# Performance work log

Hardware: AMD Instinct MI355X
Metric: run time of the kernel (lower is better)

The kernel has to match this reference:

```python
import jax, jax.numpy as jnp
import numpy as np

GROUPS = 8
EPS = 1e-3  # keras GroupNormalization default epsilon


def group_norm(x, gamma, beta):
    # x: [B, H, W, C], channels-last, normalize over (H, W, C//G) per group
    B, H, W, C = x.shape
    g = x.reshape(B, H, W, GROUPS, C // GROUPS)
    mean = g.mean(axis=(1, 2, 4), keepdims=True)
    var = g.var(axis=(1, 2, 4), keepdims=True)
    g = (g - mean) * jax.lax.rsqrt(var + EPS)
    return g.reshape(B, H, W, C) * gamma + beta


def setup_inputs() -> dict:
    key = jax.random.key(0)
    ks = jax.random.split(key, 6)
    B, H, W, C = 4, 64, 64, 256
    s = 1.0 / np.sqrt(C)
    return {
        "x": jax.random.normal(ks[0], (B, H, W, C), jnp.float32),
        "gn_gamma": jnp.ones((C,), jnp.float32),
        "gn_beta": jnp.zeros((C,), jnp.float32),
        "Wq": jax.random.normal(ks[1], (C, C), jnp.float32) * s,
        "bq": jnp.zeros((C,), jnp.float32),
        "Wk": jax.random.normal(ks[2], (C, C), jnp.float32) * s,
        "bk": jnp.zeros((C,), jnp.float32),
        "Wv": jax.random.normal(ks[3], (C, C), jnp.float32) * s,
        "bv": jnp.zeros((C,), jnp.float32),
        "Wp": jax.random.normal(ks[4], (C, C), jnp.float32) * s,
        "bp": jnp.zeros((C,), jnp.float32),
    }


def reference(x, gn_gamma, gn_beta, Wq, bq, Wk, bk, Wv, bv, Wp, bp):
    B, H, W, C = x.shape
    scale = jnp.float32(C) ** -0.5
    xn = group_norm(x, gn_gamma, gn_beta)  # note: residual uses NORMALIZED input (as in source)
    xf = xn.reshape(B, H * W, C)           # flatten spatial -> [B, N, C]
    q = xf @ Wq + bq
    k = xf @ Wk + bk
    v = xf @ Wv + bv
    attn = jnp.einsum('bnc,bmc->bnm', q, k) * scale  # [B, N, N]
    attn = jax.nn.softmax(attn, axis=-1)
    out = jnp.einsum('bnm,bmc->bnc', attn, v)
    out = out @ Wp + bp
    return xn + out.reshape(B, H, W, C)
```

## Files before the change

kernel.cpp:

```cpp
#include <hip/hip_runtime.h>
#include <hip/hip_bf16.h>

typedef __bf16 bf16x8 __attribute__((ext_vector_type(8)));
typedef __bf16 bf16x4 __attribute__((ext_vector_type(4)));
typedef float f32x4 __attribute__((ext_vector_type(4)));
typedef float f32x16 __attribute__((ext_vector_type(16)));

#define MFMA16(a,b,c) __builtin_amdgcn_mfma_f32_16x16x32_bf16((a),(b),(c),0,0,0)
#define MFMA32(a,b,c) __builtin_amdgcn_mfma_f32_32x32x16_bf16((a),(b),(c),0,0,0)

__device__ __forceinline__ void gload_lds16(const void* g, void* l) {
    __builtin_amdgcn_global_load_lds((const __attribute__((address_space(1))) unsigned int*)g,
                                     (__attribute__((address_space(3))) unsigned int*)l, 16, 0, 0);
}

__global__ __launch_bounds__(256) void gn_stats1(const float* __restrict__ x,
                                                 float* __restrict__ pstats) {
    int blk = blockIdx.x;
    int bg = blk >> 4, sl = blk & 15;
    int b = bg >> 3, g = bg & 7;
    const float* base = x + ((size_t)b * 4096 + sl * 256) * 256 + g * 32;
    float s = 0.f, s2 = 0.f;
    for (int i = threadIdx.x; i < 2048; i += 256) {
        int pos = i >> 3, f4 = i & 7;
        float4 v = *(const float4*)(base + (size_t)pos * 256 + f4 * 4);
        s  += v.x + v.y + v.z + v.w;
        s2 += v.x * v.x + v.y * v.y + v.z * v.z + v.w * v.w;
    }
    for (int off = 32; off; off >>= 1) {
        s  += __shfl_down(s, off);
        s2 += __shfl_down(s2, off);
    }
    __shared__ float red[8];
    int wave = threadIdx.x >> 6, lane = threadIdx.x & 63;
    if (lane == 0) { red[wave] = s; red[4 + wave] = s2; }
    __syncthreads();
    if (threadIdx.x == 0) {
        pstats[blk * 2]     = red[0] + red[1] + red[2] + red[3];
        pstats[blk * 2 + 1] = red[4] + red[5] + red[6] + red[7];
    }
}

__global__ void gn_stats2(const float* __restrict__ pstats, float* __restrict__ stats) {
    int bg = threadIdx.x;
    if (bg < 32) {
        float S = 0.f, S2 = 0.f;
        for (int sl = 0; sl < 16; sl++) {
            S  += pstats[(bg * 16 + sl) * 2];
            S2 += pstats[(bg * 16 + sl) * 2 + 1];
        }
        const float invN = 1.f / 131072.f;
        float mean = S * invN;
        float var = S2 * invN - mean * mean;
        stats[bg * 2] = mean;
        stats[bg * 2 + 1] = rsqrtf(var + 1e-3f);
    }
}

__global__ __launch_bounds__(256) void gn_norm(const float* __restrict__ x,
                                               const float* __restrict__ gamma,
                                               const float* __restrict__ beta,
                                               const float* __restrict__ stats,
                                               float* __restrict__ xn_f32,
                                               __bf16* __restrict__ xn_bf) {
    size_t idx = (size_t)blockIdx.x * 256 + threadIdx.x;
    int c4 = (int)(idx & 63);
    int row = (int)(idx >> 6);
    int b = row >> 12;
    int g = c4 >> 3;
    float mean = stats[(b * 8 + g) * 2];
    float rstd = stats[(b * 8 + g) * 2 + 1];
    float4 xv = ((const float4*)x)[idx];
    float4 ga = ((const float4*)gamma)[c4];
    float4 be = ((const float4*)beta)[c4];
    float4 r;
    r.x = (xv.x - mean) * rstd * ga.x + be.x;
    r.y = (xv.y - mean) * rstd * ga.y + be.y;
    r.z = (xv.z - mean) * rstd * ga.z + be.z;
    r.w = (xv.w - mean) * rstd * ga.w + be.w;
    ((float4*)xn_f32)[idx] = r;
    bf16x4 o;
    o[0] = (__bf16)r.x; o[1] = (__bf16)r.y; o[2] = (__bf16)r.z; o[3] = (__bf16)r.w;
    *(bf16x4*)(xn_bf + idx * 4) = o;
}

__global__ __launch_bounds__(256) void prep_w(const float* __restrict__ Wq,
                                              const float* __restrict__ Wk,
                                              const float* __restrict__ Wv,
                                              const float* __restrict__ Wp,
                                              __bf16* __restrict__ wt) {
    int o = blockIdx.x * 256 + threadIdx.x;
    int w = o >> 16;
    int rem = o & 65535;
    int nt   = rem >> 12;
    int kf   = (rem >> 9) & 7;
    int quad = (rem >> 7) & 3;
    int l16  = (rem >> 3) & 15;
    int j    = rem & 7;
    int n = nt * 16 + l16;
    int k = kf * 32 + quad * 8 + j;
    const float* W = (w == 0) ? Wq : (w == 1) ? Wk : (w == 2) ? Wv : Wp;
    wt[o] = (__bf16)W[k * 256 + n];
}

__global__ __launch_bounds__(128, 2) void qkv_gemm(const __bf16* __restrict__ xn,
                                                   const __bf16* __restrict__ wt,
                                                   const float* __restrict__ bq,
                                                   const float* __restrict__ bk,
                                                   const float* __restrict__ bv,
                                                   __bf16* __restrict__ qout,
                                                   __bf16* __restrict__ kout,
                                                   __bf16* __restrict__ vtout) {
    __shared__ __bf16 atile[64][264];
    int w = blockIdx.z;
    const __bf16* Wl = wt + (size_t)w * 65536;
    int tid = threadIdx.x;
    int wave = tid >> 6, lane = tid & 63;
    int quad = lane >> 4, l16 = lane & 15;
    int m0 = blockIdx.x * 64;
    int ntbase = blockIdx.y * 8 + wave * 4;

#pragma unroll
    for (int i = 0; i < 16; i++) {
        int c = tid + 128 * i;
        int row = c >> 5, col = (c & 31) * 8;
        *(bf16x8*)&atile[row][col] = *(const bf16x8*)(xn + (size_t)(m0 + row) * 256 + col);
    }
    bf16x8 bfr[4][8];
#pragma unroll
    for (int ct = 0; ct < 4; ct++)
#pragma unroll
        for (int kf = 0; kf < 8; kf++)
            bfr[ct][kf] = *(const bf16x8*)(Wl + ((((size_t)(ntbase + ct) * 8 + kf) * 4 + quad) * 16 + l16) * 8);
    __syncthreads();

    f32x4 acc[4][4];
#pragma unroll
    for (int mt = 0; mt < 4; mt++)
#pragma unroll
        for (int ct = 0; ct < 4; ct++)
#pragma unroll
            for (int r = 0; r < 4; r++) acc[mt][ct][r] = 0.f;
#pragma unroll
    for (int kf = 0; kf < 8; kf++) {
        bf16x8 af[4];
#pragma unroll
        for (int mt = 0; mt < 4; mt++)
            af[mt] = *(const bf16x8*)&atile[mt * 16 + l16][kf * 32 + quad * 8];
#pragma unroll
        for (int mt = 0; mt < 4; mt++)
#pragma unroll
            for (int ct = 0; ct < 4; ct++)
                acc[mt][ct] = MFMA16(af[mt], bfr[ct][kf], acc[mt][ct]);
    }

    if (w == 2) {
        __syncthreads();
        __bf16 (*vtl)[70] = (__bf16(*)[70])atile;
#pragma unroll
        for (int mt = 0; mt < 4; mt++) {
#pragma unroll
            for (int ct = 0; ct < 4; ct++) {
                int cl = (wave * 4 + ct) * 16 + l16;
                float bias_v = bv[blockIdx.y * 128 + cl];
                bf16x4 pv;
#pragma unroll
                for (int r = 0; r < 4; r++) pv[r] = (__bf16)(acc[mt][ct][r] + bias_v);
                *(bf16x4*)&vtl[cl][mt * 16 + quad * 4] = pv;
            }
        }
        __syncthreads();
        int bb = m0 >> 12, n0g = m0 & 4095;
#pragma unroll
        for (int j = 0; j < 8; j++) {
            int chunk = tid + 128 * j;
            int cl = chunk >> 3, n8 = chunk & 7;
            *(bf16x8*)(vtout + ((size_t)(bb * 256 + blockIdx.y * 128 + cl)) * 4096 + n0g + n8 * 8)
                = *(const bf16x8*)&vtl[cl][n8 * 8];
        }
    } else {
        const float* bias = (w == 0) ? bq : bk;
        const float qscale = 0.09016844f;
#pragma unroll
        for (int mt = 0; mt < 4; mt++) {
#pragma unroll
            for (int ct = 0; ct < 4; ct++) {
                int c = (ntbase + ct) * 16 + l16;
                float bias_v = bias[c];
#pragma unroll
                for (int r = 0; r < 4; r++) {
                    int m = m0 + mt * 16 + quad * 4 + r;
                    float val = acc[mt][ct][r] + bias_v;
                    if (w == 0) qout[(size_t)m * 256 + c] = (__bf16)(val * qscale);
                    else        kout[(size_t)m * 256 + c] = (__bf16)val;
                }
            }
        }
    }
}

__global__ __launch_bounds__(256, 2) void flash_attn(const __bf16* __restrict__ q,
                                                     const __bf16* __restrict__ k,
                                                     const __bf16* __restrict__ vt,
                                                     __bf16* __restrict__ po,
                                                     float* __restrict__ ml) {
    __shared__ __align__(16) char smem[69632];
    __bf16 (*vtile0)[36] = (__bf16(*)[36])(smem + 32768);
    __bf16 (*vtile1)[36] = (__bf16(*)[36])(smem + 51200);
    __bf16 (*otr)[32][264] = (__bf16(*)[32][264])smem;

    const int tid = threadIdx.x;
    const int wave = tid >> 6, lane = tid & 63;
    const int l32 = lane & 31, h = lane >> 5;
    const int fid = blockIdx.x;
    const int cid = ((fid & 7) << 6) | (fid >> 3);
    const int qt  = cid & 31;
    const int ksb = cid >> 5;
    const int ks  = ksb & 3, b = ksb >> 2;
    const int row0 = qt * 128 + wave * 32;
    const size_t rowg0 = (size_t)b * 4096 + row0;

    const char*   kb = (const char*)(k + ((size_t)b * 4096 + ks * 1024) * 256);
    const __bf16* vb = vt + (size_t)b * 256 * 4096 + ks * 1024;

    int koff[4];
#pragma unroll
    for (int i = 0; i < 4; i++) {
        int P = wave * 256 + i * 64 + lane;
        int r = P >> 5, cp = P & 31;
        koff[i] = r * 512 + (cp ^ r) * 16;
    }
    const int kldsoff = wave * 4096;

    bf16x8 qf[16];
    const __bf16* qbase = q + (rowg0 + l32) * 256 + h * 8;
#pragma unroll
    for (int s = 0; s < 16; s++) qf[s] = *(const bf16x8*)(qbase + s * 16);

    f32x16 acc[8];
#pragma unroll
    for (int ct = 0; ct < 8; ct++)
#pragma unroll
        for (int r = 0; r < 16; r++) acc[ct][r] = 0.f;
    float mi = -1e30f, li = 0.f;

    const int vr_ = tid >> 2, vc4 = tid & 3;

#pragma unroll
    for (int i = 0; i < 4; i++)
        gload_lds16(kb + koff[i], smem + kldsoff + i * 1024);
    {
        bf16x8 vc[4];
#pragma unroll
        for (int i = 0; i < 4; i++)
            vc[i] = *(const bf16x8*)(vb + (size_t)(vr_ + 64 * i) * 4096 + vc4 * 8);
#pragma unroll
        for (int i = 0; i < 4; i++)
            *(bf16x8*)&vtile0[vr_ + 64 * i][vc4 * 8] = vc[i];
    }
    __syncthreads();

    for (int it = 0; it < 32; ++it) {
        const int cur = it & 1;
        char* kcur = smem + (cur ? 16384 : 0);
        char* knxt = smem + (cur ? 0 : 16384);
        __bf16 (*vcur)[36] = cur ? vtile1 : vtile0;
        __bf16 (*vnxt)[36] = cur ? vtile0 : vtile1;

        bf16x8 vc[4];
        if (it + 1 < 32) {
            const char* kg = kb + (size_t)(it + 1) * 16384;
#pragma unroll
            for (int i = 0; i < 4; i++)
                gload_lds16(kg + koff[i], knxt + kldsoff + i * 1024);
            const int kn = (it + 1) * 32;
#pragma unroll
            for (int i = 0; i < 4; i++)
                vc[i] = *(const bf16x8*)(vb + (size_t)(vr_ + 64 * i) * 4096 + kn + vc4 * 8);
        }

        f32x16 s;
#pragma unroll
        for (int r = 0; r < 16; r++) s[r] = 0.f;
#pragma unroll
        for (int kf = 0; kf < 16; kf++) {
            int cl = kf * 2 + h;
            bf16x8 ka = *(const bf16x8*)(kcur + l32 * 512 + ((cl ^ l32) << 4));
            s = MFMA32(ka, qf[kf], s);
        }
        float mx = s[0];
#pragma unroll
        for (int r = 1; r < 16; r++) mx = fmaxf(mx, s[r]);
        mx = fmaxf(mx, __shfl_xor(mx, 32));
        if (__ballot(mx > mi + 8.0f)) {
            float mnew = fmaxf(mi, mx);
            float alpha = exp2f(mi - mnew);
#pragma unroll
            for (int ct = 0; ct < 8; ct++)
#pragma unroll
                for (int r = 0; r < 16; r++) acc[ct][r] *= alpha;
            li *= alpha;
            mi = mnew;
        }
        float rs = 0.f;
#pragma unroll
        for (int r = 0; r < 16; r++) { float p = exp2f(s[r] - mi); s[r] = p; rs += p; }
        rs += __shfl_xor(rs, 32);
        li += rs;
        bf16x8 pf0, pf1;
#pragma unroll
        for (int j = 0; j < 8; j++) { pf0[j] = (__bf16)s[j]; pf1[j] = (__bf16)s[8 + j]; }
        if (it + 1 < 32) {
#pragma unroll
            for (int i = 0; i < 4; i++)
                *(bf16x8*)&vnxt[vr_ + 64 * i][vc4 * 8] = vc[i];
        }
#pragma unroll
        for (int ct = 0; ct < 8; ct++) {
            const __bf16* vr = &vcur[ct * 32 + l32][0];
            bf16x4 a00 = *(const bf16x4*)(vr + 4 * h);
            bf16x4 a01 = *(const bf16x4*)(vr + 8 + 4 * h);
            bf16x8 va0 = __builtin_shufflevector(a00, a01, 0, 1, 2, 3, 4, 5, 6, 7);
            acc[ct] = MFMA32(va0, pf0, acc[ct]);
            bf16x4 a10 = *(const bf16x4*)(vr + 16 + 4 * h);
            bf16x4 a11 = *(const bf16x4*)(vr + 24 + 4 * h);
            bf16x8 va1 = __builtin_shufflevector(a10, a11, 0, 1, 2, 3, 4, 5, 6, 7);
            acc[ct] = MFMA32(va1, pf1, acc[ct]);
        }
        __syncthreads();
    }

#pragma unroll
    for (int ct = 0; ct < 8; ct++) {
#pragma unroll
        for (int pk = 0; pk < 4; pk++) {
            bf16x4 op;
            op[0] = (__bf16)acc[ct][pk * 4];     op[1] = (__bf16)acc[ct][pk * 4 + 1];
            op[2] = (__bf16)acc[ct][pk * 4 + 2]; op[3] = (__bf16)acc[ct][pk * 4 + 3];
            *(bf16x4*)&otr[wave][l32][ct * 32 + pk * 8 + h * 4] = op;
        }
    }
    if (lane < 32) {
        float2 v; v.x = mi; v.y = li;
        *(float2*)&ml[((size_t)ks * 16384 + rowg0 + l32) * 2] = v;
    }
    __syncthreads();
    __bf16* pobase = po + ((size_t)ks * 16384 + rowg0) * 256;
    const int rr = lane >> 1, half = lane & 1;
#pragma unroll
    for (int j = 0; j < 16; j++) {
        bf16x8 val = *(const bf16x8*)&otr[wave][rr][half * 128 + j * 8];
        *(bf16x8*)(pobase + (size_t)rr * 256 + half * 128 + j * 8) = val;
    }
}

__global__ __launch_bounds__(128, 2) void proj_gemm(const __bf16* __restrict__ po,
                                                    const float* __restrict__ ml,
                                                    const __bf16* __restrict__ wpl,
                                                    const float* __restrict__ bp,
                                                    float* __restrict__ out) {
    __shared__ __bf16 atile[64][264];
    int tid = threadIdx.x;
    int wave = tid >> 6, lane = tid & 63;
    int quad = lane >> 4, l16 = lane & 15;
    int m0 = blockIdx.x * 64;
    int ntbase = blockIdx.y * 8 + wave * 4;

#pragma unroll
    for (int i = 0; i < 16; i++) {
        int c = tid + 128 * i;
        int row = c >> 5, col8 = c & 31;
        int m = m0 + row;
        float mm[4], ll[4];
#pragma unroll
        for (int s = 0; s < 4; s++) {
            float2 v = *(const float2*)&ml[((size_t)s * 16384 + m) * 2];
            mm[s] = v.x; ll[s] = v.y;
        }
        float M = fmaxf(fmaxf(mm[0], mm[1]), fmaxf(mm[2], mm[3]));
        float den = 0.f, w[4];
#pragma unroll
        for (int s = 0; s < 4; s++) { w[s] = exp2f(mm[s] - M); den += ll[s] * w[s]; }
        float accv[8];
#pragma unroll
        for (int e = 0; e < 8; e++) accv[e] = 0.f;
#pragma unroll
        for (int s = 0; s < 4; s++) {
            bf16x8 pv = *(const bf16x8*)(po + ((size_t)s * 16384 + m) * 256 + col8 * 8);
#pragma unroll
            for (int e = 0; e < 8; e++) accv[e] += w[s] * (float)pv[e];
        }
        float rinv = 1.f / den;
        bf16x8 o;
#pragma unroll
        for (int e = 0; e < 8; e++) o[e] = (__bf16)(accv[e] * rinv);
        *(bf16x8*)&atile[row][col8 * 8] = o;
    }
    bf16x8 bfr[4][8];
#pragma unroll
    for (int ct = 0; ct < 4; ct++)
#pragma unroll
        for (int kf = 0; kf < 8; kf++)
            bfr[ct][kf] = *(const bf16x8*)(wpl + ((((size_t)(ntbase + ct) * 8 + kf) * 4 + quad) * 16 + l16) * 8);
    __syncthreads();

    f32x4 acc[4][4];
#pragma unroll
    for (int mt = 0; mt < 4; mt++)
#pragma unroll
        for (int ct = 0; ct < 4; ct++)
#pragma unroll
            for (int r = 0; r < 4; r++) acc[mt][ct][r] = 0.f;
#pragma unroll
    for (int kf = 0; kf < 8; kf++) {
        bf16x8 af[4];
#pragma unroll
        for (int mt = 0; mt < 4; mt++)
            af[mt] = *(const bf16x8*)&atile[mt * 16 + l16][kf * 32 + quad * 8];
#pragma unroll
        for (int mt = 0; mt < 4; mt++)
#pragma unroll
            for (int ct = 0; ct < 4; ct++)
                acc[mt][ct] = MFMA16(af[mt], bfr[ct][kf], acc[mt][ct]);
    }
#pragma unroll
    for (int mt = 0; mt < 4; mt++) {
#pragma unroll
        for (int ct = 0; ct < 4; ct++) {
            int c = (ntbase + ct) * 16 + l16;
            float bias_v = bp[c];
#pragma unroll
            for (int r = 0; r < 4; r++) {
                int m = m0 + mt * 16 + quad * 4 + r;
                size_t idx = (size_t)m * 256 + c;
                out[idx] = out[idx] + acc[mt][ct][r] + bias_v;
            }
        }
    }
}

extern "C" void kernel_launch(void* const* d_in, const int* in_sizes, int n_in,
                              void* d_out, int out_size, void* d_ws, size_t ws_size,
                              hipStream_t stream) {
    const float* x     = (const float*)d_in[0];
    const float* gamma = (const float*)d_in[1];
    const float* beta  = (const float*)d_in[2];
    const float* Wq    = (const float*)d_in[3];
    const float* bq    = (const float*)d_in[4];
    const float* Wk    = (const float*)d_in[5];
    const float* bk    = (const float*)d_in[6];
    const float* Wv    = (const float*)d_in[7];
    const float* bv    = (const float*)d_in[8];
    const float* Wp    = (const float*)d_in[9];
    const float* bp    = (const float*)d_in[10];
    float* out = (float*)d_out;

    char* ws = (char*)d_ws;
    __bf16* xn_bf   = (__bf16*)(ws);
    __bf16* wt      = (__bf16*)(ws + 8388608);
    __bf16* qbuf    = (__bf16*)(ws + 8912896);
    __bf16* kbuf    = (__bf16*)(ws + 17301504);
    __bf16* vtbuf   = (__bf16*)(ws + 25690112);
    __bf16* po      = (__bf16*)(ws + 34078720);
    float*  ml      = (float*)(ws + 67633152);
    float*  pstats  = (float*)(ws + 68157440);
    float*  gstats  = (float*)(ws + 68161536);

    gn_stats1<<<512, 256, 0, stream>>>(x, pstats);
    gn_stats2<<<1, 64, 0, stream>>>(pstats, gstats);
    gn_norm<<<4096, 256, 0, stream>>>(x, gamma, beta, gstats, out, xn_bf);
    prep_w<<<1024, 256, 0, stream>>>(Wq, Wk, Wv, Wp, wt);
    qkv_gemm<<<dim3(256, 2, 3), 128, 0, stream>>>(xn_bf, wt, bq, bk, bv, qbuf, kbuf, vtbuf);
    flash_attn<<<512, 256, 0, stream>>>(qbuf, kbuf, vtbuf, po, ml);
    proj_gemm<<<dim3(256, 2), 128, 0, stream>>>(po, ml, wt + 3 * 65536, bp, out);
}
```

Measured before the change: 256.1 us.

## Restructure flash attention into 512-thread blocks with async K/V LDS pipeline

The flash attention kernel now runs 8 waves per block, so each block covers 256 query rows and K/V tiles are shared by twice as many waves. V is loaded straight into swizzled LDS with global_load_lds instead of going through registers. Loads run two 32-key tiles ahead in a double-buffered epoch scheme, with one barrier per two tiles. The QK dot product is split into two independent MFMA chains, and s_setprio is raised around the PV MFMAs. The kernel uses 132 KB of dynamic shared memory, which cuts occupancy to one block per CU and halves the grid to 256 blocks. That risks underfilling the 256 CUs and exposing more latency.

```diff
diff --git a/kernel.cpp b/kernel.cpp
--- a/kernel.cpp
+++ b/kernel.cpp
@@ -199,38 +199,44 @@
     }
 }
 
-__global__ __launch_bounds__(256, 2) void flash_attn(const __bf16* __restrict__ q,
+__global__ __launch_bounds__(512, 2) void flash_attn(const __bf16* __restrict__ q,
                                                      const __bf16* __restrict__ k,
                                                      const __bf16* __restrict__ vt,
                                                      __bf16* __restrict__ po,
                                                      float* __restrict__ ml) {
-    __shared__ __align__(16) char smem[69632];
-    __bf16 (*vtile0)[36] = (__bf16(*)[36])(smem + 32768);
-    __bf16 (*vtile1)[36] = (__bf16(*)[36])(smem + 51200);
+    extern __shared__ __align__(16) char smem[];
     __bf16 (*otr)[32][264] = (__bf16(*)[32][264])smem;
 
     const int tid = threadIdx.x;
     const int wave = tid >> 6, lane = tid & 63;
     const int l32 = lane & 31, h = lane >> 5;
     const int fid = blockIdx.x;
-    const int cid = ((fid & 7) << 6) | (fid >> 3);
-    const int qt  = cid & 31;
-    const int ksb = cid >> 5;
+    const int cid = ((fid & 7) << 5) | (fid >> 3);
+    const int qt  = cid & 15;
+    const int ksb = cid >> 4;
     const int ks  = ksb & 3, b = ksb >> 2;
-    const int row0 = qt * 128 + wave * 32;
+    const int row0 = qt * 256 + wave * 32;
     const size_t rowg0 = (size_t)b * 4096 + row0;
 
     const char*   kb = (const char*)(k + ((size_t)b * 4096 + ks * 1024) * 256);
     const __bf16* vb = vt + (size_t)b * 256 * 4096 + ks * 1024;
 
-    int koff[4];
-#pragma unroll
-    for (int i = 0; i < 4; i++) {
-        int P = wave * 256 + i * 64 + lane;
+    int koff[2];
+#pragma unroll
+    for (int i = 0; i < 2; i++) {
+        int P = i * 512 + tid;
         int r = P >> 5, cp = P & 31;
         koff[i] = r * 512 + (cp ^ r) * 16;
     }
-    const int kldsoff = wave * 4096;
+    int voff[2];
+#pragma unroll
+    for (int i = 0; i < 2; i++) {
+        int P = i * 512 + tid;
+        int ch = P >> 2, c4 = P & 3;
+        int sw = (ch ^ (ch >> 2)) & 3;
+        voff[i] = ch * 4096 + (c4 ^ sw) * 8;
+    }
+    const int sbase = wave * 1024;
 
     bf16x8 qf[16];
     const __bf16* qbase = q + (rowg0 + l32) * 256 + h * 8;
@@ -244,91 +250,104 @@
         for (int r = 0; r < 16; r++) acc[ct][r] = 0.f;
     float mi = -1e30f, li = 0.f;
 
-    const int vr_ = tid >> 2, vc4 = tid & 3;
-
-#pragma unroll
-    for (int i = 0; i < 4; i++)
-        gload_lds16(kb + koff[i], smem + kldsoff + i * 1024);
-    {
-        bf16x8 vc[4];
-#pragma unroll
-        for (int i = 0; i < 4; i++)
-            vc[i] = *(const bf16x8*)(vb + (size_t)(vr_ + 64 * i) * 4096 + vc4 * 8);
-#pragma unroll
-        for (int i = 0; i < 4; i++)
-            *(bf16x8*)&vtile0[vr_ + 64 * i][vc4 * 8] = vc[i];
-    }
-    __syncthreads();
-
-    for (int it = 0; it < 32; ++it) {
-        const int cur = it & 1;
-        char* kcur = smem + (cur ? 16384 : 0);
-        char* knxt = smem + (cur ? 0 : 16384);
-        __bf16 (*vcur)[36] = cur ? vtile1 : vtile0;
-        __bf16 (*vnxt)[36] = cur ? vtile0 : vtile1;
-
-        bf16x8 vc[4];
-        if (it + 1 < 32) {
-            const char* kg = kb + (size_t)(it + 1) * 16384;
-#pragma unroll
-            for (int i = 0; i < 4; i++)
-                gload_lds16(kg + koff[i], knxt + kldsoff + i * 1024);
-            const int kn = (it + 1) * 32;
-#pragma unroll
-            for (int i = 0; i < 4; i++)
-                vc[i] = *(const bf16x8*)(vb + (size_t)(vr_ + 64 * i) * 4096 + kn + vc4 * 8);
-        }
-
-        f32x16 s;
-#pragma unroll
-        for (int r = 0; r < 16; r++) s[r] = 0.f;
-#pragma unroll
-        for (int kf = 0; kf < 16; kf++) {
-            int cl = kf * 2 + h;
-            bf16x8 ka = *(const bf16x8*)(kcur + l32 * 512 + ((cl ^ l32) << 4));
-            s = MFMA32(ka, qf[kf], s);
-        }
-        float mx = s[0];
-#pragma unroll
-        for (int r = 1; r < 16; r++) mx = fmaxf(mx, s[r]);
-        mx = fmaxf(mx, __shfl_xor(mx, 32));
-        if (__ballot(mx > mi + 8.0f)) {
-            float mnew = fmaxf(mi, mx);
-            float alpha = exp2f(mi - mnew);
-#pragma unroll
-            for (int ct = 0; ct < 8; ct++)
-#pragma unroll
-                for (int r = 0; r < 16; r++) acc[ct][r] *= alpha;
-            li *= alpha;
-            mi = mnew;
-        }
-        float rs = 0.f;
-#pragma unroll
-        for (int r = 0; r < 16; r++) { float p = exp2f(s[r] - mi); s[r] = p; rs += p; }
-        rs += __shfl_xor(rs, 32);
-        li += rs;
-        bf16x8 pf0, pf1;
-#pragma unroll
-        for (int j = 0; j < 8; j++) { pf0[j] = (__bf16)s[j]; pf1[j] = (__bf16)s[8 + j]; }
-        if (it + 1 < 32) {
-#pragma unroll
-            for (int i = 0; i < 4; i++)
-                *(bf16x8*)&vnxt[vr_ + 64 * i][vc4 * 8] = vc[i];
-        }
-#pragma unroll
-        for (int ct = 0; ct < 8; ct++) {
-            const __bf16* vr = &vcur[ct * 32 + l32][0];
-            bf16x4 a00 = *(const bf16x4*)(vr + 4 * h);
-            bf16x4 a01 = *(const bf16x4*)(vr + 8 + 4 * h);
-            bf16x8 va0 = __builtin_shufflevector(a00, a01, 0, 1, 2, 3, 4, 5, 6, 7);
-            acc[ct] = MFMA32(va0, pf0, acc[ct]);
-            bf16x4 a10 = *(const bf16x4*)(vr + 16 + 4 * h);
-            bf16x4 a11 = *(const bf16x4*)(vr + 24 + 4 * h);
-            bf16x8 va1 = __builtin_shufflevector(a10, a11, 0, 1, 2, 3, 4, 5, 6, 7);
-            acc[ct] = MFMA32(va1, pf1, acc[ct]);
-        }
-        __syncthreads();
-    }
+#pragma unroll
+    for (int t = 0; t < 2; t++)
+#pragma unroll
+        for (int i = 0; i < 2; i++)
+            gload_lds16(kb + t * 16384 + koff[i], smem + t * 16384 + i * 8192 + sbase);
+#pragma unroll
+    for (int t = 0; t < 2; t++)
+#pragma unroll
+        for (int i = 0; i < 2; i++)
+            gload_lds16(vb + t * 32 + voff[i], smem + 65536 + t * 16384 + i * 8192 + sbase);
+    asm volatile("s_waitcnt vmcnt(0)" ::: "memory");
+    __builtin_amdgcn_sched_barrier(0);
+    __builtin_amdgcn_s_barrier();
+
+#define FA_TILE(KCUR, VCUR)                                                          \
+  {                                                                                  \
+    const char* kcur_ = (KCUR);                                                      \
+    const char* vcur_ = (VCUR);                                                      \
+    f32x16 s0_, s1_;                                                                 \
+    _Pragma("unroll") for (int r = 0; r < 16; r++) { s0_[r] = 0.f; s1_[r] = 0.f; }   \
+    _Pragma("unroll") for (int u = 0; u < 8; u++) {                                  \
+      { int cl = 2 * u + h;                                                          \
+        bf16x8 ka = *(const bf16x8*)(kcur_ + l32 * 512 + ((cl ^ l32) << 4));         \
+        s0_ = MFMA32(ka, qf[u], s0_); }                                              \
+      { int cl = 2 * (u + 8) + h;                                                    \
+        bf16x8 ka = *(const bf16x8*)(kcur_ + l32 * 512 + ((cl ^ l32) << 4));         \
+        s1_ = MFMA32(ka, qf[u + 8], s1_); }                                          \
+    }                                                                                \
+    _Pragma("unroll") for (int r = 0; r < 16; r++) s0_[r] += s1_[r];                 \
+    float mx = s0_[0];                                                               \
+    _Pragma("unroll") for (int r = 1; r < 16; r++) mx = fmaxf(mx, s0_[r]);           \
+    mx = fmaxf(mx, __shfl_xor(mx, 32));                                              \
+    if (__ballot(mx > mi + 8.0f)) {                                                  \
+      float mnew = fmaxf(mi, mx);                                                    \
+      float alpha = exp2f(mi - mnew);                                                \
+      _Pragma("unroll") for (int ct = 0; ct < 8; ct++)                               \
+        _Pragma("unroll") for (int r = 0; r < 16; r++) acc[ct][r] *= alpha;          \
+      li *= alpha; mi = mnew;                                                        \
+    }                                                                                \
+    float rs = 0.f;                                                                  \
+    _Pragma("unroll") for (int r = 0; r < 16; r++) {                                 \
+      float p = exp2f(s0_[r] - mi); s0_[r] = p; rs += p; }                           \
+    rs += __shfl_xor(rs, 32);                                                        \
+    li += rs;                                                                        \
+    bf16x8 pf0, pf1;                                                                 \
+    _Pragma("unroll") for (int j = 0; j < 8; j++) {                                  \
+      pf0[j] = (__bf16)s0_[j]; pf1[j] = (__bf16)s0_[8 + j]; }                        \
+    {                                                                                \
+      const int sb = ((l32 ^ (l32 >> 2)) & 3) << 4;                                  \
+      const char* vrow = vcur_ + l32 * 64 + h * 8;                                   \
+      __builtin_amdgcn_s_setprio(1);                                                 \
+      _Pragma("unroll") for (int ct = 0; ct < 8; ct++) {                             \
+        const char* vr2 = vrow + ct * 2048;                                          \
+        bf16x4 a00 = *(const bf16x4*)(vr2 + sb);                                     \
+        bf16x4 a01 = *(const bf16x4*)(vr2 + (sb ^ 16));                              \
+        bf16x8 va0 = __builtin_shufflevector(a00, a01, 0, 1, 2, 3, 4, 5, 6, 7);      \
+        acc[ct] = MFMA32(va0, pf0, acc[ct]);                                         \
+        bf16x4 a10 = *(const bf16x4*)(vr2 + (sb ^ 32));                              \
+        bf16x4 a11 = *(const bf16x4*)(vr2 + (sb ^ 48));                              \
+        bf16x8 va1 = __builtin_shufflevector(a10, a11, 0, 1, 2, 3, 4, 5, 6, 7);      \
+        acc[ct] = MFMA32(va1, pf1, acc[ct]);                                         \
+      }                                                                              \
+      __builtin_amdgcn_s_setprio(0);                                                 \
+    }                                                                                \
+  }
+
+#define FA_EPOCH(E, P, STG)                                                          \
+  {                                                                                  \
+    const int e_ = (E);                                                              \
+    if (STG) {                                                                       \
+      const char* kg_ = kb + (size_t)(2 * e_ + 2) * 16384;                           \
+      char* kd_ = smem + ((P) ? 0 : 32768);                                          \
+      _Pragma("unroll") for (int t = 0; t < 2; t++)                                  \
+        _Pragma("unroll") for (int i = 0; i < 2; i++)                                \
+          gload_lds16(kg_ + t * 16384 + koff[i], kd_ + t * 16384 + i * 8192 + sbase);\
+    }                                                                                \
+    FA_TILE(smem + ((P) ? 32768 : 0), smem + 65536 + ((P) ? 32768 : 0));             \
+    if (STG) {                                                                       \
+      const int kn_ = (2 * e_ + 2) * 32;                                             \
+      char* vd_ = smem + 65536 + ((P) ? 0 : 32768);                                  \
+      _Pragma("unroll") for (int t = 0; t < 2; t++)                                  \
+        _Pragma("unroll") for (int i = 0; i < 2; i++)                                \
+          gload_lds16(vb + kn_ + t * 32 + voff[i], vd_ + t * 16384 + i * 8192 + sbase);\
+    }                                                                                \
+    FA_TILE(smem + ((P) ? 32768 : 0) + 16384, smem + 65536 + ((P) ? 32768 : 0) + 16384);\
+    asm volatile("s_waitcnt vmcnt(0) lgkmcnt(0)" ::: "memory");                      \
+    __builtin_amdgcn_sched_barrier(0);                                               \
+    __builtin_amdgcn_s_barrier();                                                    \
+  }
+
+    for (int ee = 0; ee < 7; ++ee) {
+        FA_EPOCH(2 * ee,     0, 1);
+        FA_EPOCH(2 * ee + 1, 1, 1);
+    }
+    FA_EPOCH(14, 0, 1);
+    FA_EPOCH(15, 1, 0);
+#undef FA_EPOCH
+#undef FA_TILE
 
 #pragma unroll
     for (int ct = 0; ct < 8; ct++) {
@@ -466,11 +485,18 @@
     float*  pstats  = (float*)(ws + 68157440);
     float*  gstats  = (float*)(ws + 68161536);
 
+    static bool attr_set = false;
+    if (!attr_set) {
+        hipFuncSetAttribute((const void*)flash_attn,
+                            hipFuncAttributeMaxDynamicSharedMemorySize, 135168);
+        attr_set = true;
+    }
+
     gn_stats1<<<512, 256, 0, stream>>>(x, pstats);
     gn_stats2<<<1, 64, 0, stream>>>(pstats, gstats);
     gn_norm<<<4096, 256, 0, stream>>>(x, gamma, beta, gstats, out, xn_bf);
     prep_w<<<1024, 256, 0, stream>>>(Wq, Wk, Wv, Wp, wt);
     qkv_gemm<<<dim3(256, 2, 3), 128, 0, stream>>>(xn_bf, wt, bq, bk, bv, qbuf, kbuf, vtbuf);
-    flash_attn<<<512, 256, 0, stream>>>(qbuf, kbuf, vtbuf, po, ml);
+    flash_attn<<<256, 512, 135168, stream>>>(qbuf, kbuf, vtbuf, po, ml);
     proj_gemm<<<dim3(256, 2), 128, 0, stream>>>(po, ml, wt + 3 * 65536, bp, out);
 }
```

New measurement: 267.6 us. 1.04x slower.
